# Kernel tuning notes

Measured on AMD Instinct MI355X. Metric: run time of the kernel, lower is better.

The kernel has to match this reference:

```python
import jax, jax.numpy as jnp
import numpy as np

H = 12          # heads (longformer-base)
DH = 64         # head dim
W = 256         # one-sided window (attention_window=512 in HF convention)


def _heads(t, B, S):
    return t.reshape(B, S, H, DH).transpose(0, 2, 1, 3)  # [B,H,S,dh]


def _forward(x, mask, clss, emb, pos, wq, wk, wv, wo, wqg, wkg, wvg):
    B, S = x.shape
    D = emb.shape[1]
    h = emb[x] + pos[None, :S]                      # [B,S,D]

    scale = DH ** -0.5
    q = _heads(h @ wq, B, S) * scale                # [B,H,S,dh]
    k = _heads(h @ wk, B, S)
    v = _heads(h @ wv, B, S)

    # ---- sliding-window (banded) attention, chunked like HF ----
    nc = S // W
    kpos = (jnp.arange(nc) * W - W)[:, None] + jnp.arange(3 * W)[None, :]   # [nc,3w] absolute key pos
    kidx = kpos + W                                  # index into padded seq
    kp = jnp.pad(k, ((0, 0), (0, 0), (W, W), (0, 0)))
    vp = jnp.pad(v, ((0, 0), (0, 0), (W, W), (0, 0)))
    Kc = kp[:, :, kidx, :]                           # [B,H,nc,3w,dh]
    Vc = vp[:, :, kidx, :]
    Qc = q.reshape(B, H, nc, W, DH)
    band = jnp.einsum('bhcqd,bhckd->bhcqk', Qc, Kc)  # [B,H,nc,w,3w]

    qpos = (jnp.arange(nc) * W)[:, None] + jnp.arange(W)[None, :]           # [nc,w]
    rel = kpos[:, None, :] - qpos[:, :, None]                               # [nc,w,3w]
    inband = (rel >= -W) & (rel <= W) & (kpos[:, None, :] >= 0) & (kpos[:, None, :] < S)

    is_global = jnp.zeros((S,), bool).at[clss].set(True)
    kpos_c = jnp.clip(kpos, 0, S - 1)
    # global keys are handled via dedicated columns, so remove them from the band (as HF does)
    key_ok = (mask[:, kpos_c] != 0) & (~is_global[kpos_c])                  # [B,nc,3w]

    NEG = jnp.finfo(band.dtype).min
    m = inband[None, None] & key_ok[:, None, :, None, :]                    # [B,H,nc,w,3w]
    band = jnp.where(m, band, NEG)
    band_flat = band.reshape(B, H, S, 3 * W)

    # ---- local queries attending to global keys ----
    kg_loc = k[:, :, clss, :]                        # [B,H,G,dh]
    vg_loc = v[:, :, clss, :]
    sg = jnp.einsum('bhsd,bhgd->bhsg', q, kg_loc)
    gm = (mask[:, clss] != 0)[:, None, None, :]
    sg = jnp.where(gm, sg, NEG)

    scores = jnp.concatenate([band_flat, sg], axis=-1)   # [B,H,S,3w+G]
    probs = jax.nn.softmax(scores, axis=-1)
    p_band = probs[..., : 3 * W].reshape(B, H, nc, W, 3 * W)
    p_g = probs[..., 3 * W:]
    out = jnp.einsum('bhcqk,bhckd->bhcqd', p_band, Vc).reshape(B, H, S, DH)
    out = out + jnp.einsum('bhsg,bhgd->bhsd', p_g, vg_loc)

    # ---- global queries: full attention with separate global projections ----
    qg = _heads(h @ wqg, B, S)[:, :, clss, :] * scale    # [B,H,G,dh]
    kg = _heads(h @ wkg, B, S)
    vg = _heads(h @ wvg, B, S)
    sgg = jnp.einsum('bhgd,bhsd->bhgs', qg, kg)
    sgg = jnp.where((mask != 0)[:, None, None, :], sgg, NEG)
    og = jnp.einsum('bhgs,bhsd->bhgd', jax.nn.softmax(sgg, axis=-1), vg)
    out = out.at[:, :, clss, :].set(og)

    top_vec = out.transpose(0, 2, 1, 3).reshape(B, S, D) @ wo
    return top_vec


def setup_inputs() -> dict:
    key = jax.random.key(0)
    ks = jax.random.split(key, 12)
    B, S, D, V, G = 2, 4096, 768, 50265, 64
    std = 0.02
    x = jax.random.randint(ks[0], (B, S), 0, V)
    mask = jnp.ones((B, S), jnp.int32)
    clss = jnp.sort(jax.random.randint(ks[1], (G,), 0, S))
    emb = jax.random.normal(ks[2], (V, D), jnp.float32) * std
    pos = jax.random.normal(ks[3], (S, D), jnp.float32) * std
    wq = jax.random.normal(ks[4], (D, D), jnp.float32) * std
    wk = jax.random.normal(ks[5], (D, D), jnp.float32) * std
    wv = jax.random.normal(ks[6], (D, D), jnp.float32) * std
    wo = jax.random.normal(ks[7], (D, D), jnp.float32) * std
    wqg = jax.random.normal(ks[8], (D, D), jnp.float32) * std
    wkg = jax.random.normal(ks[9], (D, D), jnp.float32) * std
    wvg = jax.random.normal(ks[10], (D, D), jnp.float32) * std
    return {"x": x, "mask": mask, "clss": clss, "emb": emb, "pos": pos,
            "wq": wq, "wk": wk, "wv": wv, "wo": wo,
            "wqg": wqg, "wkg": wkg, "wvg": wvg}


def reference(x, mask, clss, emb, pos, wq, wk, wv, wo, wqg, wkg, wvg):
    return _forward(x, mask, clss, emb, pos, wq, wk, wv, wo, wqg, wkg, wvg)
```

## Files before the change

kernel.cpp:

```cpp
#include <hip/hip_runtime.h>
#include <stdint.h>

typedef unsigned short u16;
typedef unsigned char u8;
typedef unsigned int u32;
typedef __attribute__((ext_vector_type(8))) short short8x;
typedef __attribute__((ext_vector_type(4))) float f32x4;
typedef __attribute__((ext_vector_type(16))) float f32x16;

#define DEV static __device__ __forceinline__

DEV u16 f2bf(float f) {
  union { float f; unsigned u; } v; v.f = f;
  unsigned r = v.u + 0x7FFFu + ((v.u >> 16) & 1u);
  return (u16)(r >> 16);
}
DEV int imin(int a, int b) { return a < b ? a : b; }
DEV int imax(int a, int b) { return a > b ? a : b; }
DEV float ex2(float x) { return __builtin_exp2f(x); }

DEV void gload16(const void* g, void* l) {
  __builtin_amdgcn_global_load_lds((const __attribute__((address_space(1))) void*)g,
                                   (__attribute__((address_space(3))) void*)l, 16, 0, 0);
}

DEV u32 cvtpk_bf16(float lo, float hi) {
  u32 r;
  asm("v_cvt_pk_bf16_f32 %0, %1, %2" : "=v"(r) : "v"(lo), "v"(hi));
  return r;
}
DEV void plswap(u32& a, u32& b) {
  asm("v_permlane32_swap_b32 %0, %1" : "+v"(a), "+v"(b));
}

#define LOG2E 1.44269504f

struct WPtrs { const float* p[7]; };

__global__ __launch_bounds__(256) void prep_kernel(
    WPtrs wp, const int* __restrict__ x, const float* __restrict__ emb,
    const float* __restrict__ pos, const int* __restrict__ clss,
    const int* __restrict__ mask, u16* __restrict__ wt, u16* __restrict__ hb,
    u16* __restrict__ hg, u32* __restrict__ kv32, u32* __restrict__ mv32,
    u32* __restrict__ mc32) {
  __shared__ __align__(16) char smraw[64 * 72 * 4];
  const int bid = blockIdx.x;
  const int t = threadIdx.x;

  if (bid < 1008) {
    const int mat = bid / 144;
    const int inner = bid - mat * 144;
    const int kt = inner % 12, nt = inner / 12;
    const float* __restrict__ w = wp.p[mat];
    float(*tile)[72] = (float(*)[72])smraw;
    {
      const int kk = t >> 2, n0 = (t & 3) * 16;
      const float* src = w + (size_t)(kt * 64 + kk) * 768 + nt * 64 + n0;
#pragma unroll
      for (int i = 0; i < 4; ++i)
        *(float4*)&tile[kk][n0 + i * 4] = *(const float4*)(src + i * 4);
    }
    __syncthreads();
    {
      const int nn = t >> 2, k0 = (t & 3) * 16;
      u16* dst = wt + (size_t)(mat * 768 + nt * 64 + nn) * 768 + kt * 64 + k0;
      short8x v0, v1;
#pragma unroll
      for (int j = 0; j < 8; ++j) {
        v0[j] = (short)f2bf(tile[k0 + j][nn]);
        v1[j] = (short)f2bf(tile[k0 + 8 + j][nn]);
      }
      *(short8x*)dst = v0;
      *(short8x*)(dst + 8) = v1;
    }
    return;
  }
  if (bid < 2032) {
    const int vb = bid - 1008;
    const int n4 = 2 * 4096 * 192;
    for (int i = vb * 256 + t; i < n4; i += 1024 * 256) {
      const int r = i / 192;
      const int d4 = i - r * 192;
      const int s = r & 4095;
      const int tok = x[r];
      const float4 e = *(const float4*)(emb + (size_t)tok * 768 + d4 * 4);
      const float4 p = *(const float4*)(pos + (size_t)s * 768 + d4 * 4);
      union { u16 u[4]; uint2 v; } o;
      o.u[0] = f2bf(e.x + p.x);
      o.u[1] = f2bf(e.y + p.y);
      o.u[2] = f2bf(e.z + p.z);
      o.u[3] = f2bf(e.w + p.w);
      *(uint2*)(hb + (size_t)r * 768 + d4 * 4) = o.v;
    }
    return;
  }
  if (bid == 2032) {
    u8* isg = (u8*)smraw;
    for (int i = t; i < 4096; i += 256) isg[i] = 0;
    __syncthreads();
    if (t < 64) isg[clss[t]] = 1;
    __syncthreads();
    {
      const int b = t >> 7, i = t & 127;
      u32 kv = 0, mvv = 0;
      for (int j = 0; j < 32; ++j) {
        const int key = i * 32 + j;
        const u32 m = (u32)(mask[b * 4096 + key] != 0);
        mvv |= m << j;
        kv |= (m & (u32)(isg[key] == 0)) << j;
      }
      kv32[b * 128 + i] = kv;
      mv32[b * 128 + i] = mvv;
    }
    if (t < 4) {
      const int b = t >> 1, wi = t & 1;
      u32 mc = 0;
      for (int j = 0; j < 32; ++j) {
        const int g = wi * 32 + j;
        mc |= (u32)(mask[b * 4096 + clss[g]] != 0) << j;
      }
      mc32[b * 2 + wi] = mc;
    }
    return;
  }
  {
    const int i = (bid - 2033) * 256 + t;
    const int r = i / 192, d4 = i - r * 192;
    const int b = r >> 6, g = r & 63;
    const int s = clss[g];
    const int tok = x[b * 4096 + s];
    const float4 e = *(const float4*)(emb + (size_t)tok * 768 + d4 * 4);
    const float4 p = *(const float4*)(pos + (size_t)s * 768 + d4 * 4);
    union { u16 u[4]; uint2 v; } o;
    o.u[0] = f2bf(e.x + p.x);
    o.u[1] = f2bf(e.y + p.y);
    o.u[2] = f2bf(e.z + p.z);
    o.u[3] = f2bf(e.w + p.w);
    *(uint2*)(hg + (size_t)r * 768 + d4 * 4) = o.v;
  }
}

struct Outs6 { u16* p[6]; };

template <int MODE>
__global__ __launch_bounds__(256) void gemm_kernel(const u16* __restrict__ A, const u16* __restrict__ Bt,
                                                   const u16* __restrict__ A2, const u16* __restrict__ Bt2,
                                                   Outs6 outs, float* __restrict__ outF) {
  __shared__ __align__(16) u16 smA[2][128 * 64];
  __shared__ __align__(16) u16 smB[2][128 * 64];
  const int t = threadIdx.x;
  const int l = t & 63, w = t >> 6;
  const int l15 = l & 15, grp = l >> 4;
  const int wm = w >> 1, wn = w & 1;
  int bx = blockIdx.x, by = blockIdx.y;
  bool qg = false;
  if (MODE == 0) {
    int id = blockIdx.x;
    if (id >= 1920) {
      qg = true;
      bx = id - 1920;
      by = 0;
    } else {
      id = (id & 7) * 240 + (id >> 3);
      bx = id % 30;
      by = id / 30;
    }
  }
  const u16* __restrict__ Ap = (MODE == 0 && qg) ? A2 : A;
  const u16* __restrict__ Btp = (MODE == 0 && qg) ? Bt2 : Bt;
  const int m0 = by * 128, n0 = bx * 128;
  const f32x4 zero4 = {0.f, 0.f, 0.f, 0.f};
  f32x4 acc[4][4];
#pragma unroll
  for (int mi = 0; mi < 4; ++mi)
#pragma unroll
    for (int ni = 0; ni < 4; ++ni) acc[mi][ni] = zero4;

  const int sr = l >> 3;
  const int scb = (l & 7) * 16;

  auto STAGE = [&](int kb, int d) {
#pragma unroll
    for (int c = 0; c < 4; ++c) {
      const int rg = w * 4 + c;
      const int r = rg * 8 + sr;
      const int sc = scb ^ (((r >> 2) & 3) << 5);
      gload16(Ap + (size_t)(m0 + r) * 768 + kb * 64 + (sc >> 1), (char*)smA[d] + rg * 1024);
      gload16(Btp + (size_t)(n0 + r) * 768 + kb * 64 + (sc >> 1), (char*)smB[d] + rg * 1024);
    }
  };
  const int xorf = ((l15 >> 2) & 3) << 5;
  auto RDA = [&](int d, int mi, int kk) {
    return *(const short8x*)((const char*)smA[d] + (wm * 64 + mi * 16 + l15) * 128 + ((kk * 64 + grp * 16) ^ xorf));
  };
  auto RDB = [&](int d, int ni, int kk) {
    return *(const short8x*)((const char*)smB[d] + (wn * 64 + ni * 16 + l15) * 128 + ((kk * 64 + grp * 16) ^ xorf));
  };

  STAGE(0, 0);
  STAGE(1, 1);
  asm volatile("s_waitcnt vmcnt(8)" ::: "memory");
  __builtin_amdgcn_s_barrier();
  __builtin_amdgcn_sched_barrier(0);

  short8x a0[4], b0[4], a1[4], b1[4];
#pragma unroll
  for (int i = 0; i < 4; ++i) { a0[i] = RDA(0, i, 0); b0[i] = RDB(0, i, 0); }

  for (int kt = 0; kt < 12; ++kt) {
    const int cur = kt & 1;
#pragma unroll
    for (int i = 0; i < 4; ++i) { a1[i] = RDA(cur, i, 1); b1[i] = RDB(cur, i, 1); }
    __builtin_amdgcn_s_setprio(1);
#pragma unroll
    for (int mi = 0; mi < 4; ++mi)
#pragma unroll
      for (int ni = 0; ni < 4; ++ni)
        acc[mi][ni] = __builtin_amdgcn_mfma_f32_16x16x32_bf16(a0[mi], b0[ni], acc[mi][ni], 0, 0, 0);
    __builtin_amdgcn_s_setprio(0);
    if (kt < 11) {
      asm volatile("s_waitcnt lgkmcnt(0)" ::: "memory");
      __builtin_amdgcn_s_barrier();
      __builtin_amdgcn_sched_barrier(0);
      if (kt < 10) {
        STAGE(kt + 2, cur);
        asm volatile("s_waitcnt vmcnt(8)" ::: "memory");
      } else {
        asm volatile("s_waitcnt vmcnt(0)" ::: "memory");
      }
      __builtin_amdgcn_s_barrier();
      __builtin_amdgcn_sched_barrier(0);
#pragma unroll
      for (int i = 0; i < 4; ++i) { a0[i] = RDA(cur ^ 1, i, 0); b0[i] = RDB(cur ^ 1, i, 0); }
    }
    __builtin_amdgcn_s_setprio(1);
#pragma unroll
    for (int mi = 0; mi < 4; ++mi)
#pragma unroll
      for (int ni = 0; ni < 4; ++ni)
        acc[mi][ni] = __builtin_amdgcn_mfma_f32_16x16x32_bf16(a1[mi], b1[ni], acc[mi][ni], 0, 0, 0);
    __builtin_amdgcn_s_setprio(0);
  }

  if (MODE == 0) {
    if (qg) {
      u16* __restrict__ base = outs.p[5];
#pragma unroll
      for (int mi = 0; mi < 4; ++mi)
#pragma unroll
        for (int ni = 0; ni < 4; ++ni) {
          const int col = n0 + wn * 64 + ni * 16 + l15;
          const int hd = col >> 6, dh = col & 63;
#pragma unroll
          for (int rr = 0; rr < 4; ++rr) {
            const int row = wm * 64 + mi * 16 + grp * 4 + rr;
            const int b = row >> 6, g = row & 63;
            base[((size_t)(b * 12 + hd) * 64 + g) * 64 + dh] = f2bf(acc[mi][ni][rr] * 0.125f * LOG2E);
          }
        }
      return;
    }
    const int mat = bx / 6;
    const int inn0 = n0 - mat * 768 + wn * 64;
    u16* __restrict__ base = outs.p[mat];
    if (mat == 2 || mat == 4) {
#pragma unroll
      for (int mi = 0; mi < 4; ++mi) {
        const int row0 = m0 + wm * 64 + mi * 16 + grp * 4;
        const int b = row0 >> 12, s = row0 & 4095;
#pragma unroll
        for (int ni = 0; ni < 4; ++ni) {
          const int col = inn0 + ni * 16 + l15;
          const int hd = col >> 6, dh = col & 63;
          union { u16 u[4]; uint2 v; } o;
#pragma unroll
          for (int rr = 0; rr < 4; ++rr) o.u[rr] = f2bf(acc[mi][ni][rr]);
          *(uint2*)(base + ((size_t)(b * 12 + hd) * 64 + dh) * 4096 + s) = o.v;
        }
      }
    } else {
      const float scl = (mat == 0) ? 0.125f * LOG2E : 1.0f;
#pragma unroll
      for (int mi = 0; mi < 4; ++mi)
#pragma unroll
        for (int ni = 0; ni < 4; ++ni) {
          const int col = inn0 + ni * 16 + l15;
          const int hd = col >> 6, dh = col & 63;
#pragma unroll
          for (int rr = 0; rr < 4; ++rr) {
            const int row = m0 + wm * 64 + mi * 16 + grp * 4 + rr;
            const int b = row >> 12, s = row & 4095;
            base[((size_t)(b * 12 + hd) * 4096 + s) * 64 + dh] = f2bf(acc[mi][ni][rr] * scl);
          }
        }
    }
  } else {
#pragma unroll
    for (int mi = 0; mi < 4; ++mi)
#pragma unroll
      for (int rr = 0; rr < 4; ++rr) {
        const int row = m0 + wm * 64 + mi * 16 + grp * 4 + rr;
#pragma unroll
        for (int ni = 0; ni < 4; ++ni) {
          const int col = n0 + wn * 64 + ni * 16 + l15;
          outF[(size_t)row * 768 + col] = acc[mi][ni][rr];
        }
      }
  }
}

__global__ __launch_bounds__(256) void gcls_kernel(const u16* __restrict__ kB, const u16* __restrict__ vTs,
                                                   const int* __restrict__ clss,
                                                   u16* __restrict__ kcls, u16* __restrict__ vtcls) {
  const int bh = blockIdx.x;
  __shared__ int sc[64];
  const int t = threadIdx.x;
  if (t < 64) sc[t] = clss[t];
  __syncthreads();
  {
    const int g = t >> 2, d0 = (t & 3) * 16;
    const int row = sc[g];
    const u16* pk = kB + ((size_t)bh * 4096 + row) * 64 + d0;
    u16* ok = kcls + ((size_t)bh * 64 + g) * 64 + d0;
    *(short8x*)ok = *(const short8x*)pk;
    *(short8x*)(ok + 8) = *(const short8x*)(pk + 8);
  }
  {
    const int dh = t >> 2, g0 = (t & 3) * 16;
    const u16* vrow = vTs + ((size_t)bh * 64 + dh) * 4096;
    short8x v0, v1;
#pragma unroll
    for (int j = 0; j < 8; ++j) {
      v0[j] = (short)vrow[sc[g0 + j]];
      v1[j] = (short)vrow[sc[g0 + 8 + j]];
    }
    u16* o = vtcls + ((size_t)bh * 64 + dh) * 64 + g0;
    *(short8x*)o = v0;
    *(short8x*)(o + 8) = v1;
  }
}

struct AttnState {
  f32x16 a0, a1;
  float m, l;
};

#define ATTN_SOFTMAX_PV(S, s0, s1, vm0, vm1, LOADV0, LOADV1)                        \
  {                                                                                  \
    float mx[8];                                                                     \
    _Pragma("unroll") for (int e = 0; e < 8; ++e)                                    \
        mx[e] = fmaxf(fmaxf(s0[e], s0[e + 8]), fmaxf(s1[e], s1[e + 8]));             \
    mx[0] = fmaxf(mx[0], mx[4]); mx[1] = fmaxf(mx[1], mx[5]);                        \
    mx[2] = fmaxf(mx[2], mx[6]); mx[3] = fmaxf(mx[3], mx[7]);                        \
    mx[0] = fmaxf(mx[0], mx[2]); mx[1] = fmaxf(mx[1], mx[3]);                        \
    float mv = fmaxf(mx[0], mx[1]);                                                  \
    mv = fmaxf(mv, __shfl_xor(mv, 32));                                              \
    if (!__all(mv <= S.m + 8.f)) {                                                   \
      const float mn = fmaxf(S.m, mv);                                               \
      const float sc = ex2(S.m - mn);                                                \
      S.m = mn; S.l *= sc;                                                           \
      _Pragma("unroll") for (int e = 0; e < 16; ++e) { S.a0[e] *= sc; S.a1[e] *= sc; } \
    }                                                                                \
    float p0[16], p1[16];                                                            \
    if ((vm0 & vm1) == 0xFFFFFFFFu) {                                                \
      _Pragma("unroll") for (int e = 0; e < 16; ++e) {                               \
        p0[e] = ex2(s0[e] - S.m); p1[e] = ex2(s1[e] - S.m);                          \
      }                                                                              \
    } else {                                                                         \
      const u32 w0 = vm0 >> (hf * 4), w1 = vm1 >> (hf * 4);                          \
      _Pragma("unroll") for (int e = 0; e < 16; ++e) {                               \
        const int cr = (e & 3) + 8 * (e >> 2);                                       \
        p0[e] = ex2(s0[e] - S.m) * (float)((w0 >> cr) & 1u);                         \
        p1[e] = ex2(s1[e] - S.m) * (float)((w1 >> cr) & 1u);                         \
      }                                                                              \
    }                                                                                \
    float sm[8];                                                                     \
    _Pragma("unroll") for (int e = 0; e < 8; ++e)                                    \
        sm[e] = (p0[e] + p0[e + 8]) + (p1[e] + p1[e + 8]);                           \
    sm[0] += sm[4]; sm[1] += sm[5]; sm[2] += sm[6]; sm[3] += sm[7];                  \
    sm[0] += sm[2]; sm[1] += sm[3];                                                  \
    float ls = sm[0] + sm[1];                                                        \
    ls += __shfl_xor(ls, 32);                                                        \
    S.l += ls;                                                                       \
    _Pragma("unroll") for (int st = 0; st < 2; ++st) {                               \
      const float* pp = st ? p1 : p0;                                                \
      _Pragma("unroll") for (int c = 0; c < 2; ++c) {                                \
        u32 A1 = cvtpk_bf16(pp[8 * c + 0], pp[8 * c + 1]);                           \
        u32 A2 = cvtpk_bf16(pp[8 * c + 2], pp[8 * c + 3]);                           \
        u32 B1 = cvtpk_bf16(pp[8 * c + 4], pp[8 * c + 5]);                           \
        u32 B2 = cvtpk_bf16(pp[8 * c + 6], pp[8 * c + 7]);                           \
        plswap(A1, B1); plswap(A2, B2);                                              \
        union { u32 w[4]; short8x v; } u;                                            \
        u.w[0] = A1; u.w[1] = A2; u.w[2] = B1; u.w[3] = B2;                          \
        const int sc4 = st * 2 + c;                                                  \
        const short8x vf0 = LOADV0(sc4);                                             \
        const short8x vf1 = LOADV1(sc4);                                             \
        S.a0 = __builtin_amdgcn_mfma_f32_32x32x16_bf16(vf0, u.v, S.a0, 0, 0, 0);     \
        S.a1 = __builtin_amdgcn_mfma_f32_32x32x16_bf16(vf1, u.v, S.a1, 0, 0, 0);     \
      }                                                                              \
    }                                                                                \
  }

DEV void attn_tile64(const u16* __restrict__ kp, const u16* __restrict__ vp, int vstr,
                     u32 vm0, u32 vm1, const short8x* qf, AttnState& S, int l31, int hf) {
  const int h8 = hf * 8;
  const f32x16 z16 = {0.f};
  f32x16 s0 = z16, s1 = z16;
  const u16* kr0 = kp + (size_t)l31 * 64 + h8;
  const u16* kr1 = kr0 + 32 * 64;
#pragma unroll
  for (int ks = 0; ks < 4; ++ks) {
    const short8x kf0 = *(const short8x*)(kr0 + ks * 16);
    const short8x kf1 = *(const short8x*)(kr1 + ks * 16);
    s0 = __builtin_amdgcn_mfma_f32_32x32x16_bf16(kf0, qf[ks], s0, 0, 0, 0);
    s1 = __builtin_amdgcn_mfma_f32_32x32x16_bf16(kf1, qf[ks], s1, 0, 0, 0);
  }
#define LV0(sc4) (*(const short8x*)(vp + (sc4) * 16 + h8 + (size_t)l31 * vstr))
#define LV1(sc4) (*(const short8x*)(vp + (sc4) * 16 + h8 + (size_t)(32 + l31) * vstr))
  ATTN_SOFTMAX_PV(S, s0, s1, vm0, vm1, LV0, LV1)
#undef LV0
#undef LV1
}

DEV void attn_tile64_lds(const char* __restrict__ Kl, const char* __restrict__ Vl,
                         u32 vm0, u32 vm1, const short8x* qf, AttnState& S, int l31, int hf) {
  const int swz = (l31 & 7) << 4;
  const f32x16 z16 = {0.f};
  f32x16 s0 = z16, s1 = z16;
#pragma unroll
  for (int ks = 0; ks < 4; ++ks) {
    const int cb = (hf * 16 + ks * 32) ^ swz;
    const short8x kf0 = *(const short8x*)(Kl + l31 * 128 + cb);
    const short8x kf1 = *(const short8x*)(Kl + (32 + l31) * 128 + cb);
    s0 = __builtin_amdgcn_mfma_f32_32x32x16_bf16(kf0, qf[ks], s0, 0, 0, 0);
    s1 = __builtin_amdgcn_mfma_f32_32x32x16_bf16(kf1, qf[ks], s1, 0, 0, 0);
  }
#define LV0(sc4) (*(const short8x*)(Vl + l31 * 128 + (((sc4) * 32 + hf * 16) ^ swz)))
#define LV1(sc4) (*(const short8x*)(Vl + (32 + l31) * 128 + (((sc4) * 32 + hf * 16) ^ swz)))
  ATTN_SOFTMAX_PV(S, s0, s1, vm0, vm1, LV0, LV1)
#undef LV0
#undef LV1
}

DEV u32 bandmask32(int q, int kb2) {
  const int lo = imax(q - 256 - kb2, 0);
  const int hi = imin(q + 256 - kb2, 31);
  if (hi < lo) return 0u;
  return (0xFFFFFFFFu << lo) & (0xFFFFFFFFu >> (31 - hi));
}

struct FusedArgs {
  const u16 *qB, *kB, *vT, *kcls, *vtcls, *qgc, *kgB, *vgT;
  const u32 *kv32, *mv32, *mc32;
  u16* aout;
  float *pm, *pl, *pacc;
};

__global__ __launch_bounds__(256, 3) void band_kernel(FusedArgs a) {
  const int t = threadIdx.x;
  const int w = t >> 6, l = t & 63;
  const int l31 = l & 31, hf = l >> 5, h4 = hf * 4;
  const f32x16 z16 = {0.f};

  __shared__ __align__(16) char Ktile[2][8192];
  __shared__ __align__(16) char Vtile[2][8192];

  if (blockIdx.x < 96) {
    const int wid = blockIdx.x * 4 + w;
    const int sl = wid & 7;
    const int qsub = (wid >> 3) & 1;
    const int bh = wid >> 4;
    const int b = bh / 12;
    const int q = qsub * 32 + l31;

    const u16* kgb = a.kgB + (size_t)bh * 4096 * 64;
    const u16* vgb = a.vgT + (size_t)bh * 64 * 4096;
    short8x qf[4];
#pragma unroll
    for (int ks = 0; ks < 4; ++ks)
      qf[ks] = *(const short8x*)(a.qgc + ((size_t)bh * 64 + q) * 64 + ks * 16 + hf * 8);

    AttnState S;
    S.a0 = z16; S.a1 = z16; S.m = -60.f; S.l = 0.f;
    for (int tt = sl * 8; tt < sl * 8 + 8; ++tt) {
      const int kb = tt * 64;
      const u32 vm0 = a.mv32[b * 128 + tt * 2];
      const u32 vm1 = a.mv32[b * 128 + tt * 2 + 1];
      attn_tile64(kgb + (size_t)kb * 64, vgb + kb, 4096, vm0, vm1, qf, S, l31, hf);
    }
    const int pbase = (bh * 8 + sl) * 64;
    float* pr = a.pacc + ((size_t)pbase + q) * 64;
#pragma unroll
    for (int rq = 0; rq < 4; ++rq) {
      f32x4 v0 = {S.a0[rq * 4 + 0], S.a0[rq * 4 + 1], S.a0[rq * 4 + 2], S.a0[rq * 4 + 3]};
      f32x4 v1 = {S.a1[rq * 4 + 0], S.a1[rq * 4 + 1], S.a1[rq * 4 + 2], S.a1[rq * 4 + 3]};
      *(f32x4*)(pr + rq * 8 + h4) = v0;
      *(f32x4*)(pr + 32 + rq * 8 + h4) = v1;
    }
    if (hf == 0) {
      a.pm[pbase + q] = S.m;
      a.pl[pbase + q] = S.l;
    }
    return;
  }

  int bid = blockIdx.x - 96;
  bid = (bid & 7) * 96 + (bid >> 3);
  const int qblk = bid & 31;
  const int h = (bid >> 5) % 12;
  const int b = bid / 384;
  const int bh = b * 12 + h;
  const int q0b = qblk * 128;
  const int q0w = q0b + w * 32;
  const int q = q0w + l31;

  const u16* kbh = a.kB + (size_t)bh * 4096 * 64;
  const u16* vbh = a.vT + (size_t)bh * 64 * 4096;
  const u16* kcb = a.kcls + (size_t)bh * 4096;
  const u16* vcb = a.vtcls + (size_t)bh * 4096;

  short8x qf[4];
#pragma unroll
  for (int ks = 0; ks < 4; ++ks)
    qf[ks] = *(const short8x*)(a.qB + ((size_t)bh * 4096 + q) * 64 + ks * 16 + hf * 8);

  AttnState S;
  S.a0 = z16; S.a1 = z16; S.m = -60.f; S.l = 0.f;

  const int tloB = imax(0, q0b - 256) >> 6;
  const int thiB = imin(63, (q0b + 383) >> 6);
  const int nB = thiB - tloB + 1;
  const int tlo_w = (imax(0, q0w - 256) >> 6) - tloB;
  const int thi_w = (imin(63, (q0w + 287) >> 6)) - tloB;

  auto STAGE = [&](const u16* ksrc, const u16* vsrc, int vstr, int buf) {
#pragma unroll
    for (int c = 0; c < 2; ++c) {
      const int rw = w + 4 * c;
      const int row = rw * 8 + (l >> 3);
      const int seg = (l & 7) ^ (row & 7);
      gload16(ksrc + (size_t)row * 64 + seg * 8, Ktile[buf] + rw * 1024);
      gload16(vsrc + (size_t)row * vstr + seg * 8, Vtile[buf] + rw * 1024);
    }
  };

  STAGE(kbh + (size_t)tloB * 64 * 64, vbh + (size_t)tloB * 64, 4096, 0);
  __syncthreads();

  for (int i = 0; i <= nB; ++i) {
    const int buf = i & 1;
    if (i < nB) {
      if (i + 1 == nB) STAGE(kcb, vcb, 64, buf ^ 1);
      else             STAGE(kbh + (size_t)(tloB + i + 1) * 64 * 64,
                             vbh + (size_t)(tloB + i + 1) * 64, 4096, buf ^ 1);
    }
    const bool isG = (i == nB);
    if (isG || (i >= tlo_w && i <= thi_w)) {
      u32 vm0, vm1;
      if (isG) {
        vm0 = a.mc32[b * 2];
        vm1 = a.mc32[b * 2 + 1];
      } else {
        const int tt = tloB + i;
        const int kb = tt * 64;
        vm0 = a.kv32[b * 128 + tt * 2];
        vm1 = a.kv32[b * 128 + tt * 2 + 1];
        const int d0 = kb - q0w, d1 = kb + 32 - q0w;
        if (d0 < -225 || d0 > 225) vm0 &= bandmask32(q, kb);
        if (d1 < -225 || d1 > 225) vm1 &= bandmask32(q, kb + 32);
      }
      attn_tile64_lds(Ktile[buf], Vtile[buf], vm0, vm1, qf, S, l31, hf);
    }
    __syncthreads();
  }

  const float inv = 1.f / S.l;
  u16* ob = a.aout + ((size_t)b * 4096 + q) * 768 + h * 64;
#pragma unroll
  for (int rq = 0; rq < 4; ++rq) {
    union { u16 s[4]; uint2 v; } o0, o1;
#pragma unroll
    for (int j = 0; j < 4; ++j) {
      o0.s[j] = f2bf(S.a0[rq * 4 + j] * inv);
      o1.s[j] = f2bf(S.a1[rq * 4 + j] * inv);
    }
    *(uint2*)(ob + rq * 8 + h4) = o0.v;
    *(uint2*)(ob + 32 + rq * 8 + h4) = o1.v;
  }
}

__global__ __launch_bounds__(256) void ogm_kernel(const float* __restrict__ pm, const float* __restrict__ pl,
                                                  const float* __restrict__ pacc, const int* __restrict__ clss,
                                                  u16* __restrict__ aout) {
  const int bh = blockIdx.x;
  const int b = bh / 12, h = bh % 12;
  const int t = threadIdx.x;
  const int r = t >> 2, cs = (t & 3) * 16;
  float mv[8];
  float M = -1e30f;
#pragma unroll
  for (int s = 0; s < 8; ++s) {
    mv[s] = pm[(bh * 8 + s) * 64 + r];
    M = fmaxf(M, mv[s]);
  }
  float L = 0.f, f[8];
#pragma unroll
  for (int s = 0; s < 8; ++s) {
    f[s] = ex2(mv[s] - M);
    L += pl[(bh * 8 + s) * 64 + r] * f[s];
  }
  float o[16];
#pragma unroll
  for (int j = 0; j < 16; ++j) o[j] = 0.f;
#pragma unroll
  for (int s = 0; s < 8; ++s) {
    const float* pr = pacc + (size_t)(bh * 8 + s) * 4096 + r * 64 + cs;
#pragma unroll
    for (int j4 = 0; j4 < 4; ++j4) {
      const float4 a = *(const float4*)(pr + j4 * 4);
      o[j4 * 4 + 0] += a.x * f[s];
      o[j4 * 4 + 1] += a.y * f[s];
      o[j4 * 4 + 2] += a.z * f[s];
      o[j4 * 4 + 3] += a.w * f[s];
    }
  }
  const float inv = 1.f / L;
  short8x v0, v1;
#pragma unroll
  for (int j = 0; j < 8; ++j) {
    v0[j] = (short)f2bf(o[j] * inv);
    v1[j] = (short)f2bf(o[8 + j] * inv);
  }
  u16* op = aout + ((size_t)b * 4096 + clss[r]) * 768 + h * 64 + cs;
  *(short8x*)op = v0;
  *(short8x*)(op + 8) = v1;
}

extern "C" void kernel_launch(void* const* d_in, const int* in_sizes, int n_in,
                              void* d_out, int out_size, void* d_ws, size_t ws_size,
                              hipStream_t stream) {
  (void)in_sizes; (void)n_in; (void)out_size; (void)ws_size;
  const int* x = (const int*)d_in[0];
  const int* mask = (const int*)d_in[1];
  const int* clss = (const int*)d_in[2];
  const float* emb = (const float*)d_in[3];
  const float* pos = (const float*)d_in[4];
  const float* wq = (const float*)d_in[5];
  const float* wk = (const float*)d_in[6];
  const float* wv = (const float*)d_in[7];
  const float* wo = (const float*)d_in[8];
  const float* wqg = (const float*)d_in[9];
  const float* wkg = (const float*)d_in[10];
  const float* wvg = (const float*)d_in[11];
  float* out = (float*)d_out;

  char* ws = (char*)d_ws;
  size_t off = 0;
  auto alloc = [&](size_t n) { char* p = ws + off; off = (off + n + 255) & ~(size_t)255; return p; };
  const size_t SZ = (size_t)2 * 12 * 4096 * 64 * 2;
  u16* hb = (u16*)alloc(SZ);
  u16* wt = (u16*)alloc((size_t)7 * 768 * 768 * 2);
  u16* qb = (u16*)alloc(SZ);
  u16* kb = (u16*)alloc(SZ);
  u16* kgb = (u16*)alloc(SZ);
  u16* vts = (u16*)alloc(SZ);
  u16* vgts = (u16*)alloc(SZ);
  u16* hg = (u16*)alloc((size_t)128 * 768 * 2);
  u16* qgc = (u16*)alloc((size_t)24 * 64 * 64 * 2);
  u16* kcls = (u16*)alloc((size_t)24 * 64 * 64 * 2);
  u16* vtcls = (u16*)alloc((size_t)24 * 64 * 64 * 2);
  u32* kv32 = (u32*)alloc(256 * 4);
  u32* mv32 = (u32*)alloc(256 * 4);
  u32* mc32 = (u32*)alloc(4 * 4);
  u16* aout = (u16*)alloc(SZ);
  float* pm = (float*)alloc((size_t)192 * 64 * 4);
  float* pl = (float*)alloc((size_t)192 * 64 * 4);
  float* pacc = (float*)alloc((size_t)192 * 4096 * 4);

  WPtrs wp;
  wp.p[0] = wq; wp.p[1] = wk; wp.p[2] = wv; wp.p[3] = wkg; wp.p[4] = wvg; wp.p[5] = wqg; wp.p[6] = wo;

  prep_kernel<<<2129, 256, 0, stream>>>(wp, x, emb, pos, clss, mask, wt, hb, hg, kv32, mv32, mc32);

  Outs6 o5;
  o5.p[0] = qb; o5.p[1] = kb; o5.p[2] = vts; o5.p[3] = kgb; o5.p[4] = vgts; o5.p[5] = qgc;
  gemm_kernel<0><<<1926, 256, 0, stream>>>(hb, wt, hg, wt + (size_t)5 * 768 * 768, o5, nullptr);

  gcls_kernel<<<24, 256, 0, stream>>>(kb, vts, clss, kcls, vtcls);

  FusedArgs fa;
  fa.qB = qb; fa.kB = kb; fa.vT = vts; fa.kcls = kcls; fa.vtcls = vtcls;
  fa.qgc = qgc; fa.kgB = kgb; fa.vgT = vgts;
  fa.kv32 = kv32; fa.mv32 = mv32; fa.mc32 = mc32;
  fa.aout = aout; fa.pm = pm; fa.pl = pl; fa.pacc = pacc;
  band_kernel<<<864, 256, 0, stream>>>(fa);

  ogm_kernel<<<24, 256, 0, stream>>>(pm, pl, pacc, clss, aout);

  Outs6 dummy = {};
  gemm_kernel<1><<<dim3(6, 64), 256, 0, stream>>>(aout, wt + (size_t)6 * 768 * 768, nullptr, nullptr, dummy, out);
}
```

Baseline: 169.5 us.

## Prefetch K/V tiles two stages ahead with fine-grained vmcnt waits

Restructures the attention loop's K/V staging from a one-ahead prefetch with full __syncthreads to a two-ahead prefetch into the double buffer. Synchronisation now uses explicit s_waitcnt vmcnt/lgkmcnt counts and raw barriers, so a tile's global loads can still be in flight while the previous tile is computed. The aim is to hide more global-to-LDS latency. In exchange it adds a second barrier per iteration and depends on exact vmcnt accounting (4 loads per stage), which is fragile.

```diff
diff --git a/kernel.cpp b/kernel.cpp
--- a/kernel.cpp
+++ b/kernel.cpp
@@ -533,7 +533,16 @@
   const int tlo_w = (imax(0, q0w - 256) >> 6) - tloB;
   const int thi_w = (imin(63, (q0w + 287) >> 6)) - tloB;
 
-  auto STAGE = [&](const u16* ksrc, const u16* vsrc, int vstr, int buf) {
+  auto STAGEi = [&](int j, int buf) {
+    const u16* ksrc;
+    const u16* vsrc;
+    int vstr;
+    if (j == nB) { ksrc = kcb; vsrc = vcb; vstr = 64; }
+    else {
+      ksrc = kbh + (size_t)(tloB + j) * 64 * 64;
+      vsrc = vbh + (size_t)(tloB + j) * 64;
+      vstr = 4096;
+    }
 #pragma unroll
     for (int c = 0; c < 2; ++c) {
       const int rw = w + 4 * c;
@@ -544,16 +553,14 @@
     }
   };
 
-  STAGE(kbh + (size_t)tloB * 64 * 64, vbh + (size_t)tloB * 64, 4096, 0);
-  __syncthreads();
+  STAGEi(0, 0);
+  STAGEi(1, 1);
+  asm volatile("s_waitcnt vmcnt(4)" ::: "memory");
+  __builtin_amdgcn_s_barrier();
+  __builtin_amdgcn_sched_barrier(0);
 
   for (int i = 0; i <= nB; ++i) {
     const int buf = i & 1;
-    if (i < nB) {
-      if (i + 1 == nB) STAGE(kcb, vcb, 64, buf ^ 1);
-      else             STAGE(kbh + (size_t)(tloB + i + 1) * 64 * 64,
-                             vbh + (size_t)(tloB + i + 1) * 64, 4096, buf ^ 1);
-    }
     const bool isG = (i == nB);
     if (isG || (i >= tlo_w && i <= thi_w)) {
       u32 vm0, vm1;
@@ -571,7 +578,19 @@
       }
       attn_tile64_lds(Ktile[buf], Vtile[buf], vm0, vm1, qf, S, l31, hf);
     }
-    __syncthreads();
+    if (i < nB) {
+      asm volatile("s_waitcnt lgkmcnt(0)" ::: "memory");
+      __builtin_amdgcn_s_barrier();
+      __builtin_amdgcn_sched_barrier(0);
+      if (i + 2 <= nB) {
+        STAGEi(i + 2, buf);
+        asm volatile("s_waitcnt vmcnt(4)" ::: "memory");
+      } else {
+        asm volatile("s_waitcnt vmcnt(0)" ::: "memory");
+      }
+      __builtin_amdgcn_s_barrier();
+      __builtin_amdgcn_sched_barrier(0);
+    }
   }
 
   const float inv = 1.f / S.l;
```

After: 166.9 us. About the same (-1.5%).
